# Kernel tuning notes

Measured on AMD Instinct MI355X. Metric: run time of the kernel, lower is better.

Reference implementation:

```python
import jax, jax.numpy as jnp
import numpy as np

EPS = 1e-12

def _l2norm(v, axis=-1):
    n = jnp.sqrt(jnp.sum(v * v, axis=axis, keepdims=True))
    return v / jnp.maximum(n, EPS)

def setup_inputs() -> dict:
    key = jax.random.key(0)
    ks = jax.random.split(key, 6)
    B, S, E, A = 256, 128, 768, 30
    x = jax.random.normal(ks[0], (B, S, E), dtype=jnp.float32)
    W_att = jax.random.normal(ks[1], (E, E), dtype=jnp.float32) * (1.0 / np.sqrt(E))
    b_att = jnp.zeros((E,), dtype=jnp.float32)
    W_red = jax.random.normal(ks[2], (E, A), dtype=jnp.float32) * (1.0 / np.sqrt(E))
    b_red = jnp.zeros((A,), dtype=jnp.float32)
    aspect_W = jax.random.normal(ks[3], (A, E), dtype=jnp.float32) * (1.0 / np.sqrt(E))
    # negatives: uniform over other batch elements (multinomial on ones - eye)
    idx = jax.random.randint(ks[4], (B, 10), 0, B - 1)
    neg_idx = (idx + (idx >= jnp.arange(B)[:, None])).astype(jnp.int32)  # skip self
    return {"x": x, "W_att": W_att, "b_att": b_att, "W_red": W_red,
            "b_red": b_red, "aspect_W": aspect_W, "neg_idx": neg_idx}

def reference(x, W_att, b_att, W_red, b_red, aspect_W, neg_idx):
    # --- LuongAttention(general): query = mean over seq ---
    q = x.mean(axis=1)                                   # [B,E]
    qW = q @ W_att + b_att                               # [B,E]
    scores = jnp.einsum('bse,be->bs', x, qW)             # [B,S]
    attn = jax.nn.softmax(scores, axis=-1)
    z_s = jnp.einsum('bs,bse->be', attn, x)              # attended sentence vec [B,E]
    # --- reduction + reconstruction ---
    composition = jax.nn.softmax(z_s @ W_red + b_red, axis=-1)  # [B,A]
    reconstructed = composition @ aspect_W                      # [B,E]
    # --- max-margin loss with gathered negatives ---
    r_s = _l2norm(reconstructed)                         # F.normalize
    z_n = z_s[neg_idx]                                   # [B,10,E] gather
    pos = jnp.einsum('be,be->b', z_s, r_s)[:, None]      # [B,1]
    negs = jnp.einsum('bne,be->bn', z_n, r_s)            # [B,10]
    J = 1.0 - pos + negs
    margin_loss = jnp.mean(jnp.maximum(J, 0.0))
    # --- orthogonal regularization on aspect embeddings ---
    T_n = _l2norm(aspect_W, axis=1)                      # [A,E]
    G = T_n @ T_n.T - jnp.eye(aspect_W.shape[0], dtype=aspect_W.dtype)
    reg = jnp.sqrt(jnp.sum(G * G))                       # Frobenius norm
    loss = reg + margin_loss
    return (z_s, reconstructed, loss)
```

## Files before the change

kernel.cpp:

```cpp
#include <hip/hip_runtime.h>
#include <hip/hip_bf16.h>
#include <math.h>

#define B 256
#define S 128
#define E 768
#define E4 192
#define NA 30
#define NNEG 10

#define K2_KC 96
#define K2_KR 192

__device__ __forceinline__ float dot4(float4 a, float4 b) {
    return a.x * b.x + a.y * b.y + a.z * b.z + a.w * b.w;
}
__device__ __forceinline__ float wave_reduce_sum(float v) {
#pragma unroll
    for (int off = 32; off; off >>= 1) v += __shfl_down(v, off);
    return v;
}
__device__ __forceinline__ float wave_reduce_max(float v) {
#pragma unroll
    for (int off = 32; off; off >>= 1) v = fmaxf(v, __shfl_down(v, off));
    return v;
}

__global__ __launch_bounds__(768) void mean_prep_kernel(const float* __restrict__ x,
                                                        const float* __restrict__ W_red,
                                                        const float* __restrict__ aspect_W,
                                                        float* __restrict__ q,
                                                        float* __restrict__ WredT,
                                                        float* __restrict__ invn) {
    int bid = blockIdx.x;
    int tid = threadIdx.x;
    __shared__ __align__(16) float4 part[4][E4];
    __shared__ float red[12];

    if (bid < 2 * B) {
        int b = bid >> 1, half = bid & 1;
        int c = tid % E4;
        int g = tid / E4;
        const float4* xb = (const float4*)(x + (size_t)b * S * E);
        int s0 = half * 64 + g * 16;
        float4 acc = make_float4(0.f, 0.f, 0.f, 0.f);
#pragma unroll 4
        for (int s = s0; s < s0 + 16; ++s) {
            float4 v = xb[(size_t)s * E4 + c];
            acc.x += v.x; acc.y += v.y; acc.z += v.z; acc.w += v.w;
        }
        part[g][c] = acc;
        __syncthreads();
        if (tid < E4) {
            float4 a0 = part[0][c], a1 = part[1][c], a2 = part[2][c], a3 = part[3][c];
            const float inv = 1.0f / (float)S;
            float4 r;
            r.x = (a0.x + a1.x + a2.x + a3.x) * inv;
            r.y = (a0.y + a1.y + a2.y + a3.y) * inv;
            r.z = (a0.z + a1.z + a2.z + a3.z) * inv;
            r.w = (a0.w + a1.w + a2.w + a3.w) * inv;
            ((float4*)q)[((size_t)half * B + b) * E4 + c] = r;
        }
    } else {
        int a = bid - 2 * B;
        WredT[(size_t)a * E + tid] = W_red[(size_t)tid * NA + a];
        int wave = tid >> 6, lane = tid & 63;
        float v = aspect_W[(size_t)a * E + tid];
        float ss = wave_reduce_sum(v * v);
        if (lane == 0) red[wave] = ss;
        __syncthreads();
        if (tid == 0) {
            float n = 0.f;
#pragma unroll
            for (int w = 0; w < 12; ++w) n += red[w];
            invn[a] = 1.0f / fmaxf(sqrtf(n), 1e-12f);
        }
    }
}

__global__ __launch_bounds__(256) void qw_partial_kernel(const float* __restrict__ q,
                                                         const float* __restrict__ W_att,
                                                         float* __restrict__ part) {
    int b0 = blockIdx.x * 64;
    int e0 = blockIdx.y * 64;
    int kz = blockIdx.z;
    int k0 = kz * K2_KR;
    int tid = threadIdx.x;

    __shared__ __align__(16) float qs[64][K2_KC + 4];
    __shared__ __align__(16) float ws[K2_KC][64];

    int r0 = (tid >> 3) * 2;
    int c0 = (tid & 7) * 8;

    float4 a00 = make_float4(0,0,0,0), a01 = make_float4(0,0,0,0);
    float4 a10 = make_float4(0,0,0,0), a11 = make_float4(0,0,0,0);

    for (int ch = 0; ch < 2; ++ch) {
        int kc0 = k0 + ch * K2_KC;
        {
            int row = tid >> 2, ks = (tid & 3) * 24;
            const float* src0 = q + (size_t)(b0 + row) * E + kc0 + ks;
            const float* src1 = src0 + (size_t)B * E;
#pragma unroll
            for (int j = 0; j < 6; ++j) {
                float4 v0 = *(const float4*)(src0 + 4 * j);
                float4 v1 = *(const float4*)(src1 + 4 * j);
                v0.x += v1.x; v0.y += v1.y; v0.z += v1.z; v0.w += v1.w;
                *(float4*)&qs[row][ks + 4 * j] = v0;
            }
        }
        for (int i = tid; i < K2_KC * 16; i += 256) {
            int row = i >> 4, e4 = (i & 15) * 4;
            *(float4*)&ws[row][e4] =
                *(const float4*)(W_att + (size_t)(kc0 + row) * E + e0 + e4);
        }
        __syncthreads();
#pragma unroll 4
        for (int k = 0; k < K2_KC; ++k) {
            float qa = qs[r0][k], qb = qs[r0 + 1][k];
            float4 w0 = *(const float4*)&ws[k][c0];
            float4 w1 = *(const float4*)&ws[k][c0 + 4];
            a00.x += qa * w0.x; a00.y += qa * w0.y; a00.z += qa * w0.z; a00.w += qa * w0.w;
            a01.x += qa * w1.x; a01.y += qa * w1.y; a01.z += qa * w1.z; a01.w += qa * w1.w;
            a10.x += qb * w0.x; a10.y += qb * w0.y; a10.z += qb * w0.z; a10.w += qb * w0.w;
            a11.x += qb * w1.x; a11.y += qb * w1.y; a11.z += qb * w1.z; a11.w += qb * w1.w;
        }
        __syncthreads();
    }
    float* dst = part + ((size_t)kz * B + b0 + r0) * E + e0 + c0;
    *(float4*)dst = a00; *(float4*)(dst + 4) = a01;
    *(float4*)(dst + E) = a10; *(float4*)(dst + E + 4) = a11;
}

__global__ __launch_bounds__(768) void attn_ortho_kernel(const float* __restrict__ x,
                                                         const float* __restrict__ part,
                                                         const float* __restrict__ b_att,
                                                         const float* __restrict__ aspect_W,
                                                         const float* __restrict__ invn,
                                                         float* __restrict__ z_s,
                                                         float* __restrict__ Gpart) {
    int bid = blockIdx.x;
    int tid = threadIdx.x, wave = tid >> 6, lane = tid & 63;
    __shared__ __align__(16) float4 qw4[E4];
    __shared__ float att[S];
    __shared__ float red[12];
    __shared__ __align__(16) float4 zpart[4][E4];

    if (bid >= B) {
        int i = bid - B;
        float inv_i = invn[i];
        if (tid < E4) {
            float4 v = ((const float4*)aspect_W)[(size_t)i * E4 + tid];
            v.x *= inv_i; v.y *= inv_i; v.z *= inv_i; v.w *= inv_i;
            qw4[tid] = v;
        }
        __syncthreads();
        float acc = 0.f;
        for (int j = wave; j < NA; j += 12) {
            const float4* aj = (const float4*)(aspect_W + (size_t)j * E);
            float d = 0.f;
#pragma unroll
            for (int jj = 0; jj < 3; ++jj)
                d += dot4(aj[lane + 64 * jj], qw4[lane + 64 * jj]);
            d = wave_reduce_sum(d);
            if (lane == 0) {
                float g = d * invn[j] - ((i == j) ? 1.f : 0.f);
                acc += g * g;
            }
        }
        if (lane == 0) red[wave] = acc;
        __syncthreads();
        if (tid == 0) {
            float s = 0.f;
#pragma unroll
            for (int w = 0; w < 12; ++w) s += red[w];
            Gpart[i] = s;
        }
        return;
    }

    int b = bid;
    const int N4 = B * E / 4;
    if (tid < E4) {
        const float4* p = (const float4*)part;
        size_t base = (size_t)b * E4 + tid;
        float4 s0 = p[base], s1 = p[base + N4], s2 = p[base + 2 * N4], s3 = p[base + 3 * N4];
        float4 bb = ((const float4*)b_att)[tid];
        float4 r;
        r.x = s0.x + s1.x + s2.x + s3.x + bb.x;
        r.y = s0.y + s1.y + s2.y + s3.y + bb.y;
        r.z = s0.z + s1.z + s2.z + s3.z + bb.z;
        r.w = s0.w + s1.w + s2.w + s3.w + bb.w;
        qw4[tid] = r;
    }
    __syncthreads();

    const float4* xb = (const float4*)(x + (size_t)b * S * E);

    for (int p2 = wave; p2 < S / 2; p2 += 12) {
        int sA = 2 * p2;
        const float4* rA = xb + (size_t)sA * E4;
        const float4* rB = rA + E4;
        float dA = 0.f, dB = 0.f;
#pragma unroll
        for (int j = 0; j < 3; ++j) {
            float4 qv = qw4[lane + 64 * j];
            dA += dot4(rA[lane + 64 * j], qv);
            dB += dot4(rB[lane + 64 * j], qv);
        }
#pragma unroll
        for (int off = 32; off; off >>= 1) {
            dA += __shfl_down(dA, off);
            dB += __shfl_down(dB, off);
        }
        if (lane == 0) { att[sA] = dA; att[sA + 1] = dB; }
    }
    __syncthreads();

    float v = (tid < S) ? att[tid] : -3.4e38f;
    if (tid < S) {
        float m = wave_reduce_max(v);
        if (lane == 0) red[wave] = m;
    }
    __syncthreads();
    float gm = fmaxf(red[0], red[1]);
    float ex = 0.f;
    if (tid < S) {
        ex = expf(v - gm);
        float ss = wave_reduce_sum(ex);
        if (lane == 0) red[4 + wave] = ss;
    }
    __syncthreads();
    float tot = red[4] + red[5];
    if (tid < S) att[tid] = ex / tot;
    __syncthreads();

    int c = tid % E4, g = tid / E4;
    float4 acc = make_float4(0.f, 0.f, 0.f, 0.f);
#pragma unroll 4
    for (int s = g * 32 + 31; s >= g * 32; --s) {
        float w = att[s];
        float4 xv = xb[(size_t)s * E4 + c];
        acc.x += w * xv.x; acc.y += w * xv.y; acc.z += w * xv.z; acc.w += w * xv.w;
    }
    zpart[g][c] = acc;
    __syncthreads();
    if (tid < E4) {
        float4 a0 = zpart[0][tid], a1 = zpart[1][tid], a2 = zpart[2][tid], a3 = zpart[3][tid];
        float4 r;
        r.x = a0.x + a1.x + a2.x + a3.x;
        r.y = a0.y + a1.y + a2.y + a3.y;
        r.z = a0.z + a1.z + a2.z + a3.z;
        r.w = a0.w + a1.w + a2.w + a3.w;
        ((float4*)z_s)[(size_t)b * E4 + tid] = r;
    }
}

__global__ __launch_bounds__(256) void recon_margin_kernel(const float* __restrict__ z_s,
                                                           const float* __restrict__ WredT,
                                                           const float* __restrict__ b_red,
                                                           const float* __restrict__ aspect_W,
                                                           const int* __restrict__ neg_idx,
                                                           float* __restrict__ recon,
                                                           float* __restrict__ mpart) {
    int b = blockIdx.x;
    int tid = threadIdx.x, wave = tid >> 6, lane = tid & 63;
    __shared__ __align__(16) float4 z4[E4];
    __shared__ float comp[NA];
    __shared__ __align__(16) float r_sh[E];
    __shared__ float red[4];
    __shared__ float dots[12];

    if (tid < E4) z4[tid] = ((const float4*)(z_s + (size_t)b * E))[tid];
    __syncthreads();

    for (int a = wave; a < NA; a += 4) {
        const float4* wr = (const float4*)(WredT + (size_t)a * E);
        float d = 0.f;
#pragma unroll
        for (int j = 0; j < 3; ++j)
            d += dot4(wr[lane + 64 * j], z4[lane + 64 * j]);
        d = wave_reduce_sum(d);
        if (lane == 0) comp[a] = d + b_red[a];
    }
    __syncthreads();

    if (wave == 0) {
        float v = (lane < NA) ? comp[lane] : -3.4e38f;
        float m = wave_reduce_max(v);
        m = __shfl(m, 0);
        float e = (lane < NA) ? expf(v - m) : 0.f;
        float ssum = wave_reduce_sum(e);
        ssum = __shfl(ssum, 0);
        if (lane < NA) comp[lane] = e / ssum;
    }
    __syncthreads();

    float r0 = 0.f, r1 = 0.f, r2 = 0.f;
    for (int a = 0; a < NA; ++a) {
        float cm = comp[a];
        const float* ar = aspect_W + (size_t)a * E;
        r0 += cm * ar[tid];
        r1 += cm * ar[tid + 256];
        r2 += cm * ar[tid + 512];
    }
    float* rb = recon + (size_t)b * E;
    rb[tid] = r0; rb[tid + 256] = r1; rb[tid + 512] = r2;
    r_sh[tid] = r0; r_sh[tid + 256] = r1; r_sh[tid + 512] = r2;
    float sq = r0 * r0 + r1 * r1 + r2 * r2;
    sq = wave_reduce_sum(sq);
    if (lane == 0) red[wave] = sq;
    __syncthreads();
    float inv = 1.0f / fmaxf(sqrtf(red[0] + red[1] + red[2] + red[3]), 1e-12f);

    for (int d = wave; d < NNEG + 1; d += 4) {
        int row = (d == 0) ? b : neg_idx[b * NNEG + (d - 1)];
        const float4* zr = (const float4*)(z_s + (size_t)row * E);
        const float4* rr = (const float4*)r_sh;
        float acc = 0.f;
#pragma unroll
        for (int j = 0; j < 3; ++j)
            acc += dot4(zr[lane + 64 * j], rr[lane + 64 * j]);
        acc = wave_reduce_sum(acc);
        if (lane == 0) dots[d] = acc;
    }
    __syncthreads();
    if (tid == 0) {
        float pos = dots[0] * inv;
        float ssum = 0.f;
        for (int n = 1; n <= NNEG; ++n)
            ssum += fmaxf(1.f - pos + dots[n] * inv, 0.f);
        mpart[b] = ssum;
    }
}

__global__ __launch_bounds__(256) void loss_kernel(const float* __restrict__ Gpart,
                                                   const float* __restrict__ mpart,
                                                   float* __restrict__ loss_out) {
    int tid = threadIdx.x, wave = tid >> 6, lane = tid & 63;
    __shared__ float ra[4], rb[4];
    float fr = (tid < NA) ? Gpart[tid] : 0.f;
    fr = wave_reduce_sum(fr);
    if (lane == 0) ra[wave] = fr;
    float mp = mpart[tid];
    mp = wave_reduce_sum(mp);
    if (lane == 0) rb[wave] = mp;
    __syncthreads();
    if (tid == 0) {
        float frob = sqrtf(ra[0] + ra[1] + ra[2] + ra[3]);
        float msum = rb[0] + rb[1] + rb[2] + rb[3];
        loss_out[0] = frob + msum * (1.0f / (float)(B * NNEG));
    }
}

extern "C" void kernel_launch(void* const* d_in, const int* in_sizes, int n_in,
                              void* d_out, int out_size, void* d_ws, size_t ws_size,
                              hipStream_t stream) {
    const float* x        = (const float*)d_in[0];
    const float* W_att    = (const float*)d_in[1];
    const float* b_att    = (const float*)d_in[2];
    const float* W_red    = (const float*)d_in[3];
    const float* b_red    = (const float*)d_in[4];
    const float* aspect_W = (const float*)d_in[5];
    const int*   neg_idx  = (const int*)d_in[6];

    float* out   = (float*)d_out;
    float* z_s   = out;
    float* recon = out + (size_t)B * E;
    float* loss  = out + (size_t)2 * B * E;

    float* ws    = (float*)d_ws;
    float* q     = ws;
    float* part2 = q + (size_t)2 * B * E;
    float* WredT = part2 + (size_t)4 * B * E;
    float* invn  = WredT + (size_t)NA * E;
    float* Gpart = invn + 32;
    float* mpart = Gpart + 32;

    mean_prep_kernel<<<2 * B + NA, 768, 0, stream>>>(x, W_red, aspect_W, q, WredT, invn);
    qw_partial_kernel<<<dim3(4, 12, 4), 256, 0, stream>>>(q, W_att, part2);
    attn_ortho_kernel<<<B + NA, 768, 0, stream>>>(x, part2, b_att, aspect_W, invn, z_s, Gpart);
    recon_margin_kernel<<<B, 256, 0, stream>>>(z_s, WredT, b_red, aspect_W, neg_idx, recon, mpart);
    loss_kernel<<<1, 256, 0, stream>>>(Gpart, mpart, loss);
}
```

Baseline: 77.81 us.

## Fuse mean and qW GEMV into one kernel; fold loss into recon via ticket

New measurement: 126.6 us. 1.63x slower.

```diff
diff --git a/kernel.cpp b/kernel.cpp
--- a/kernel.cpp
+++ b/kernel.cpp
@@ -9,9 +9,6 @@
 #define NA 30
 #define NNEG 10
 
-#define K2_KC 96
-#define K2_KR 192
-
 __device__ __forceinline__ float dot4(float4 a, float4 b) {
     return a.x * b.x + a.y * b.y + a.z * b.z + a.w * b.w;
 }
@@ -26,43 +23,22 @@
     return v;
 }
 
-__global__ __launch_bounds__(768) void mean_prep_kernel(const float* __restrict__ x,
-                                                        const float* __restrict__ W_red,
-                                                        const float* __restrict__ aspect_W,
-                                                        float* __restrict__ q,
-                                                        float* __restrict__ WredT,
-                                                        float* __restrict__ invn) {
+__global__ __launch_bounds__(768) void meanqw_prep_kernel(const float* __restrict__ x,
+                                                          const float* __restrict__ W_att,
+                                                          const float* __restrict__ W_red,
+                                                          const float* __restrict__ aspect_W,
+                                                          float* __restrict__ part,
+                                                          float* __restrict__ WredT,
+                                                          float* __restrict__ invn,
+                                                          unsigned int* __restrict__ counter) {
     int bid = blockIdx.x;
     int tid = threadIdx.x;
-    __shared__ __align__(16) float4 part[4][E4];
+    __shared__ __align__(16) float4 qp4[4][8][24];
+    __shared__ __align__(16) float qs[8][100];
     __shared__ float red[12];
 
-    if (bid < 2 * B) {
-        int b = bid >> 1, half = bid & 1;
-        int c = tid % E4;
-        int g = tid / E4;
-        const float4* xb = (const float4*)(x + (size_t)b * S * E);
-        int s0 = half * 64 + g * 16;
-        float4 acc = make_float4(0.f, 0.f, 0.f, 0.f);
-#pragma unroll 4
-        for (int s = s0; s < s0 + 16; ++s) {
-            float4 v = xb[(size_t)s * E4 + c];
-            acc.x += v.x; acc.y += v.y; acc.z += v.z; acc.w += v.w;
-        }
-        part[g][c] = acc;
-        __syncthreads();
-        if (tid < E4) {
-            float4 a0 = part[0][c], a1 = part[1][c], a2 = part[2][c], a3 = part[3][c];
-            const float inv = 1.0f / (float)S;
-            float4 r;
-            r.x = (a0.x + a1.x + a2.x + a3.x) * inv;
-            r.y = (a0.y + a1.y + a2.y + a3.y) * inv;
-            r.z = (a0.z + a1.z + a2.z + a3.z) * inv;
-            r.w = (a0.w + a1.w + a2.w + a3.w) * inv;
-            ((float4*)q)[((size_t)half * B + b) * E4 + c] = r;
-        }
-    } else {
-        int a = bid - 2 * B;
+    if (bid >= 256) {
+        int a = bid - 256;
         WredT[(size_t)a * E + tid] = W_red[(size_t)tid * NA + a];
         int wave = tid >> 6, lane = tid & 63;
         float v = aspect_W[(size_t)a * E + tid];
@@ -75,62 +51,58 @@
             for (int w = 0; w < 12; ++w) n += red[w];
             invn[a] = 1.0f / fmaxf(sqrtf(n), 1e-12f);
         }
-    }
-}
-
-__global__ __launch_bounds__(256) void qw_partial_kernel(const float* __restrict__ q,
-                                                         const float* __restrict__ W_att,
-                                                         float* __restrict__ part) {
-    int b0 = blockIdx.x * 64;
-    int e0 = blockIdx.y * 64;
-    int kz = blockIdx.z;
-    int k0 = kz * K2_KR;
-    int tid = threadIdx.x;
-
-    __shared__ __align__(16) float qs[64][K2_KC + 4];
-    __shared__ __align__(16) float ws[K2_KC][64];
-
-    int r0 = (tid >> 3) * 2;
-    int c0 = (tid & 7) * 8;
-
-    float4 a00 = make_float4(0,0,0,0), a01 = make_float4(0,0,0,0);
-    float4 a10 = make_float4(0,0,0,0), a11 = make_float4(0,0,0,0);
-
-    for (int ch = 0; ch < 2; ++ch) {
-        int kc0 = k0 + ch * K2_KC;
-        {
-            int row = tid >> 2, ks = (tid & 3) * 24;
-            const float* src0 = q + (size_t)(b0 + row) * E + kc0 + ks;
-            const float* src1 = src0 + (size_t)B * E;
-#pragma unroll
-            for (int j = 0; j < 6; ++j) {
-                float4 v0 = *(const float4*)(src0 + 4 * j);
-                float4 v1 = *(const float4*)(src1 + 4 * j);
-                v0.x += v1.x; v0.y += v1.y; v0.z += v1.z; v0.w += v1.w;
-                *(float4*)&qs[row][ks + 4 * j] = v0;
-            }
-        }
-        for (int i = tid; i < K2_KC * 16; i += 256) {
-            int row = i >> 4, e4 = (i & 15) * 4;
-            *(float4*)&ws[row][e4] =
-                *(const float4*)(W_att + (size_t)(kc0 + row) * E + e0 + e4);
-        }
-        __syncthreads();
+        return;
+    }
+
+    if (bid == 0 && tid == 0) *counter = 0u;
+
+    int bt = bid >> 3, kt = bid & 7;
+    int b0 = bt * 8, k0 = kt * 96;
+
+    int c  = tid % 24;
+    int bi = (tid / 24) & 7;
+    int g  = tid / 192;
+    const float4* xrow = (const float4*)(x + (size_t)(b0 + bi) * S * E) + (k0 >> 2) + c;
+    float4 acc = make_float4(0.f, 0.f, 0.f, 0.f);
+#pragma unroll 8
+    for (int s = g * 32; s < g * 32 + 32; ++s) {
+        float4 v = xrow[(size_t)s * E4];
+        acc.x += v.x; acc.y += v.y; acc.z += v.z; acc.w += v.w;
+    }
+    qp4[g][bi][c] = acc;
+    __syncthreads();
+    if (tid < 192) {
+        int bj = tid / 24, cc = tid % 24;
+        float4 a0 = qp4[0][bj][cc], a1 = qp4[1][bj][cc], a2 = qp4[2][bj][cc], a3 = qp4[3][bj][cc];
+        const float inv = 1.0f / (float)S;
+        float4 r;
+        r.x = (a0.x + a1.x + a2.x + a3.x) * inv;
+        r.y = (a0.y + a1.y + a2.y + a3.y) * inv;
+        r.z = (a0.z + a1.z + a2.z + a3.z) * inv;
+        r.w = (a0.w + a1.w + a2.w + a3.w) * inv;
+        *(float4*)&qs[bj][cc * 4] = r;
+    }
+    __syncthreads();
+
+    int bj = tid / 96;
+    int e0 = (tid % 96) * 8;
+    float4 o0 = make_float4(0.f, 0.f, 0.f, 0.f), o1 = make_float4(0.f, 0.f, 0.f, 0.f);
+    const float* Wb = W_att + (size_t)k0 * E + e0;
 #pragma unroll 4
-        for (int k = 0; k < K2_KC; ++k) {
-            float qa = qs[r0][k], qb = qs[r0 + 1][k];
-            float4 w0 = *(const float4*)&ws[k][c0];
-            float4 w1 = *(const float4*)&ws[k][c0 + 4];
-            a00.x += qa * w0.x; a00.y += qa * w0.y; a00.z += qa * w0.z; a00.w += qa * w0.w;
-            a01.x += qa * w1.x; a01.y += qa * w1.y; a01.z += qa * w1.z; a01.w += qa * w1.w;
-            a10.x += qb * w0.x; a10.y += qb * w0.y; a10.z += qb * w0.z; a10.w += qb * w0.w;
-            a11.x += qb * w1.x; a11.y += qb * w1.y; a11.z += qb * w1.z; a11.w += qb * w1.w;
-        }
-        __syncthreads();
-    }
-    float* dst = part + ((size_t)kz * B + b0 + r0) * E + e0 + c0;
-    *(float4*)dst = a00; *(float4*)(dst + 4) = a01;
-    *(float4*)(dst + E) = a10; *(float4*)(dst + E + 4) = a11;
+    for (int kk = 0; kk < 24; ++kk) {
+        float4 q4 = *(const float4*)&qs[bj][kk * 4];
+#pragma unroll
+        for (int j = 0; j < 4; ++j) {
+            const float* wr = Wb + (size_t)(kk * 4 + j) * E;
+            float4 w0 = *(const float4*)wr;
+            float4 w1 = *(const float4*)(wr + 4);
+            float qv = (j == 0) ? q4.x : (j == 1) ? q4.y : (j == 2) ? q4.z : q4.w;
+            o0.x += qv * w0.x; o0.y += qv * w0.y; o0.z += qv * w0.z; o0.w += qv * w0.w;
+            o1.x += qv * w1.x; o1.y += qv * w1.y; o1.z += qv * w1.z; o1.w += qv * w1.w;
+        }
+    }
+    float* dst = part + ((size_t)kt * B + b0 + bj) * E + e0;
+    *(float4*)dst = o0; *(float4*)(dst + 4) = o1;
 }
 
 __global__ __launch_bounds__(768) void attn_ortho_kernel(const float* __restrict__ x,
@@ -185,13 +157,12 @@
     if (tid < E4) {
         const float4* p = (const float4*)part;
         size_t base = (size_t)b * E4 + tid;
-        float4 s0 = p[base], s1 = p[base + N4], s2 = p[base + 2 * N4], s3 = p[base + 3 * N4];
-        float4 bb = ((const float4*)b_att)[tid];
-        float4 r;
-        r.x = s0.x + s1.x + s2.x + s3.x + bb.x;
-        r.y = s0.y + s1.y + s2.y + s3.y + bb.y;
-        r.z = s0.z + s1.z + s2.z + s3.z + bb.z;
-        r.w = s0.w + s1.w + s2.w + s3.w + bb.w;
+        float4 r = ((const float4*)b_att)[tid];
+#pragma unroll
+        for (int i = 0; i < 8; ++i) {
+            float4 s = p[base + (size_t)i * N4];
+            r.x += s.x; r.y += s.y; r.z += s.z; r.w += s.w;
+        }
         qw4[tid] = r;
     }
     __syncthreads();
@@ -257,25 +228,29 @@
     }
 }
 
-__global__ __launch_bounds__(256) void recon_margin_kernel(const float* __restrict__ z_s,
-                                                           const float* __restrict__ WredT,
-                                                           const float* __restrict__ b_red,
-                                                           const float* __restrict__ aspect_W,
-                                                           const int* __restrict__ neg_idx,
-                                                           float* __restrict__ recon,
-                                                           float* __restrict__ mpart) {
+__global__ __launch_bounds__(768) void recon_margin_loss_kernel(const float* __restrict__ z_s,
+                                                                const float* __restrict__ WredT,
+                                                                const float* __restrict__ b_red,
+                                                                const float* __restrict__ aspect_W,
+                                                                const int* __restrict__ neg_idx,
+                                                                const float* __restrict__ Gpart,
+                                                                float* __restrict__ recon,
+                                                                float* __restrict__ mpart,
+                                                                unsigned int* __restrict__ counter,
+                                                                float* __restrict__ loss_out) {
     int b = blockIdx.x;
     int tid = threadIdx.x, wave = tid >> 6, lane = tid & 63;
     __shared__ __align__(16) float4 z4[E4];
     __shared__ float comp[NA];
     __shared__ __align__(16) float r_sh[E];
-    __shared__ float red[4];
+    __shared__ float red[12];
     __shared__ float dots[12];
+    __shared__ unsigned int ticket;
 
     if (tid < E4) z4[tid] = ((const float4*)(z_s + (size_t)b * E))[tid];
     __syncthreads();
 
-    for (int a = wave; a < NA; a += 4) {
+    for (int a = wave; a < NA; a += 12) {
         const float4* wr = (const float4*)(WredT + (size_t)a * E);
         float d = 0.f;
 #pragma unroll
@@ -297,25 +272,21 @@
     }
     __syncthreads();
 
-    float r0 = 0.f, r1 = 0.f, r2 = 0.f;
-    for (int a = 0; a < NA; ++a) {
-        float cm = comp[a];
-        const float* ar = aspect_W + (size_t)a * E;
-        r0 += cm * ar[tid];
-        r1 += cm * ar[tid + 256];
-        r2 += cm * ar[tid + 512];
-    }
-    float* rb = recon + (size_t)b * E;
-    rb[tid] = r0; rb[tid + 256] = r1; rb[tid + 512] = r2;
-    r_sh[tid] = r0; r_sh[tid + 256] = r1; r_sh[tid + 512] = r2;
-    float sq = r0 * r0 + r1 * r1 + r2 * r2;
-    sq = wave_reduce_sum(sq);
+    float r = 0.f;
+    for (int a = 0; a < NA; ++a)
+        r += comp[a] * aspect_W[(size_t)a * E + tid];
+    recon[(size_t)b * E + tid] = r;
+    r_sh[tid] = r;
+    float sq = wave_reduce_sum(r * r);
     if (lane == 0) red[wave] = sq;
     __syncthreads();
-    float inv = 1.0f / fmaxf(sqrtf(red[0] + red[1] + red[2] + red[3]), 1e-12f);
-
-    for (int d = wave; d < NNEG + 1; d += 4) {
-        int row = (d == 0) ? b : neg_idx[b * NNEG + (d - 1)];
+    float tot = 0.f;
+#pragma unroll
+    for (int w = 0; w < 12; ++w) tot += red[w];
+    float inv = 1.0f / fmaxf(sqrtf(tot), 1e-12f);
+
+    if (wave <= NNEG) {
+        int row = (wave == 0) ? b : neg_idx[b * NNEG + (wave - 1)];
         const float4* zr = (const float4*)(z_s + (size_t)row * E);
         const float4* rr = (const float4*)r_sh;
         float acc = 0.f;
@@ -323,7 +294,7 @@
         for (int j = 0; j < 3; ++j)
             acc += dot4(zr[lane + 64 * j], rr[lane + 64 * j]);
         acc = wave_reduce_sum(acc);
-        if (lane == 0) dots[d] = acc;
+        if (lane == 0) dots[wave] = acc;
     }
     __syncthreads();
     if (tid == 0) {
@@ -333,24 +304,25 @@
             ssum += fmaxf(1.f - pos + dots[n] * inv, 0.f);
         mpart[b] = ssum;
     }
-}
-
-__global__ __launch_bounds__(256) void loss_kernel(const float* __restrict__ Gpart,
-                                                   const float* __restrict__ mpart,
-                                                   float* __restrict__ loss_out) {
-    int tid = threadIdx.x, wave = tid >> 6, lane = tid & 63;
-    __shared__ float ra[4], rb[4];
-    float fr = (tid < NA) ? Gpart[tid] : 0.f;
-    fr = wave_reduce_sum(fr);
-    if (lane == 0) ra[wave] = fr;
-    float mp = mpart[tid];
-    mp = wave_reduce_sum(mp);
-    if (lane == 0) rb[wave] = mp;
-    __syncthreads();
-    if (tid == 0) {
-        float frob = sqrtf(ra[0] + ra[1] + ra[2] + ra[3]);
-        float msum = rb[0] + rb[1] + rb[2] + rb[3];
-        loss_out[0] = frob + msum * (1.0f / (float)(B * NNEG));
+
+    __threadfence();
+    if (tid == 0) ticket = atomicAdd(counter, 1u);
+    __syncthreads();
+    if (ticket == B - 1) {
+        __threadfence();
+        float mp = (tid < B) ? mpart[tid] : 0.f;
+        mp = wave_reduce_sum(mp);
+        if (lane == 0) red[wave] = mp;
+        float gp = (tid < NA) ? Gpart[tid] : 0.f;
+        gp = wave_reduce_sum(gp);
+        if (lane == 0) dots[wave] = gp;
+        __syncthreads();
+        if (tid == 0) {
+            float ms = 0.f, fr = 0.f;
+#pragma unroll
+            for (int w = 0; w < 12; ++w) { ms += red[w]; fr += dots[w]; }
+            loss_out[0] = sqrtf(fr) + ms * (1.0f / (float)(B * NNEG));
+        }
     }
 }
 
@@ -371,16 +343,16 @@
     float* loss  = out + (size_t)2 * B * E;
 
     float* ws    = (float*)d_ws;
-    float* q     = ws;
-    float* part2 = q + (size_t)2 * B * E;
-    float* WredT = part2 + (size_t)4 * B * E;
+    float* part2 = ws;
+    float* WredT = part2 + (size_t)8 * B * E;
     float* invn  = WredT + (size_t)NA * E;
     float* Gpart = invn + 32;
     float* mpart = Gpart + 32;
-
-    mean_prep_kernel<<<2 * B + NA, 768, 0, stream>>>(x, W_red, aspect_W, q, WredT, invn);
-    qw_partial_kernel<<<dim3(4, 12, 4), 256, 0, stream>>>(q, W_att, part2);
+    unsigned int* counter = (unsigned int*)(mpart + B);
+
+    meanqw_prep_kernel<<<256 + NA, 768, 0, stream>>>(x, W_att, W_red, aspect_W,
+                                                     part2, WredT, invn, counter);
     attn_ortho_kernel<<<B + NA, 768, 0, stream>>>(x, part2, b_att, aspect_W, invn, z_s, Gpart);
-    recon_margin_kernel<<<B, 256, 0, stream>>>(z_s, WredT, b_red, aspect_W, neg_idx, recon, mpart);
-    loss_kernel<<<1, 256, 0, stream>>>(Gpart, mpart, loss);
-}
+    recon_margin_loss_kernel<<<B, 768, 0, stream>>>(z_s, WredT, b_red, aspect_W, neg_idx,
+                                                    Gpart, recon, mpart, counter, loss);
+}
```

## Fuse final loss reduction into recon kernel via last-block atomic ticket

Applied to the files above, without the earlier changes.

New measurement: 122.8 us. 1.58x slower.

```diff
diff --git a/kernel.cpp b/kernel.cpp
--- a/kernel.cpp
+++ b/kernel.cpp
@@ -31,11 +31,14 @@
                                                         const float* __restrict__ aspect_W,
                                                         float* __restrict__ q,
                                                         float* __restrict__ WredT,
-                                                        float* __restrict__ invn) {
+                                                        float* __restrict__ invn,
+                                                        unsigned int* __restrict__ counter) {
     int bid = blockIdx.x;
     int tid = threadIdx.x;
     __shared__ __align__(16) float4 part[4][E4];
     __shared__ float red[12];
+
+    if (bid == 0 && tid == 0) *counter = 0u;
 
     if (bid < 2 * B) {
         int b = bid >> 1, half = bid & 1;
@@ -257,25 +260,29 @@
     }
 }
 
-__global__ __launch_bounds__(256) void recon_margin_kernel(const float* __restrict__ z_s,
-                                                           const float* __restrict__ WredT,
-                                                           const float* __restrict__ b_red,
-                                                           const float* __restrict__ aspect_W,
-                                                           const int* __restrict__ neg_idx,
-                                                           float* __restrict__ recon,
-                                                           float* __restrict__ mpart) {
+__global__ __launch_bounds__(768) void recon_margin_loss_kernel(const float* __restrict__ z_s,
+                                                                const float* __restrict__ WredT,
+                                                                const float* __restrict__ b_red,
+                                                                const float* __restrict__ aspect_W,
+                                                                const int* __restrict__ neg_idx,
+                                                                const float* __restrict__ Gpart,
+                                                                float* __restrict__ recon,
+                                                                float* __restrict__ mpart,
+                                                                unsigned int* __restrict__ counter,
+                                                                float* __restrict__ loss_out) {
     int b = blockIdx.x;
     int tid = threadIdx.x, wave = tid >> 6, lane = tid & 63;
     __shared__ __align__(16) float4 z4[E4];
     __shared__ float comp[NA];
     __shared__ __align__(16) float r_sh[E];
-    __shared__ float red[4];
+    __shared__ float red[12];
     __shared__ float dots[12];
+    __shared__ unsigned int ticket;
 
     if (tid < E4) z4[tid] = ((const float4*)(z_s + (size_t)b * E))[tid];
     __syncthreads();
 
-    for (int a = wave; a < NA; a += 4) {
+    for (int a = wave; a < NA; a += 12) {
         const float4* wr = (const float4*)(WredT + (size_t)a * E);
         float d = 0.f;
 #pragma unroll
@@ -297,25 +304,21 @@
     }
     __syncthreads();
 
-    float r0 = 0.f, r1 = 0.f, r2 = 0.f;
-    for (int a = 0; a < NA; ++a) {
-        float cm = comp[a];
-        const float* ar = aspect_W + (size_t)a * E;
-        r0 += cm * ar[tid];
-        r1 += cm * ar[tid + 256];
-        r2 += cm * ar[tid + 512];
-    }
-    float* rb = recon + (size_t)b * E;
-    rb[tid] = r0; rb[tid + 256] = r1; rb[tid + 512] = r2;
-    r_sh[tid] = r0; r_sh[tid + 256] = r1; r_sh[tid + 512] = r2;
-    float sq = r0 * r0 + r1 * r1 + r2 * r2;
-    sq = wave_reduce_sum(sq);
+    float r = 0.f;
+    for (int a = 0; a < NA; ++a)
+        r += comp[a] * aspect_W[(size_t)a * E + tid];
+    recon[(size_t)b * E + tid] = r;
+    r_sh[tid] = r;
+    float sq = wave_reduce_sum(r * r);
     if (lane == 0) red[wave] = sq;
     __syncthreads();
-    float inv = 1.0f / fmaxf(sqrtf(red[0] + red[1] + red[2] + red[3]), 1e-12f);
-
-    for (int d = wave; d < NNEG + 1; d += 4) {
-        int row = (d == 0) ? b : neg_idx[b * NNEG + (d - 1)];
+    float tot = 0.f;
+#pragma unroll
+    for (int w = 0; w < 12; ++w) tot += red[w];
+    float inv = 1.0f / fmaxf(sqrtf(tot), 1e-12f);
+
+    if (wave <= NNEG) {
+        int row = (wave == 0) ? b : neg_idx[b * NNEG + (wave - 1)];
         const float4* zr = (const float4*)(z_s + (size_t)row * E);
         const float4* rr = (const float4*)r_sh;
         float acc = 0.f;
@@ -323,7 +326,7 @@
         for (int j = 0; j < 3; ++j)
             acc += dot4(zr[lane + 64 * j], rr[lane + 64 * j]);
         acc = wave_reduce_sum(acc);
-        if (lane == 0) dots[d] = acc;
+        if (lane == 0) dots[wave] = acc;
     }
     __syncthreads();
     if (tid == 0) {
@@ -333,24 +336,25 @@
             ssum += fmaxf(1.f - pos + dots[n] * inv, 0.f);
         mpart[b] = ssum;
     }
-}
-
-__global__ __launch_bounds__(256) void loss_kernel(const float* __restrict__ Gpart,
-                                                   const float* __restrict__ mpart,
-                                                   float* __restrict__ loss_out) {
-    int tid = threadIdx.x, wave = tid >> 6, lane = tid & 63;
-    __shared__ float ra[4], rb[4];
-    float fr = (tid < NA) ? Gpart[tid] : 0.f;
-    fr = wave_reduce_sum(fr);
-    if (lane == 0) ra[wave] = fr;
-    float mp = mpart[tid];
-    mp = wave_reduce_sum(mp);
-    if (lane == 0) rb[wave] = mp;
-    __syncthreads();
-    if (tid == 0) {
-        float frob = sqrtf(ra[0] + ra[1] + ra[2] + ra[3]);
-        float msum = rb[0] + rb[1] + rb[2] + rb[3];
-        loss_out[0] = frob + msum * (1.0f / (float)(B * NNEG));
+
+    __threadfence();
+    if (tid == 0) ticket = atomicAdd(counter, 1u);
+    __syncthreads();
+    if (ticket == B - 1) {
+        __threadfence();
+        float mp = (tid < B) ? mpart[tid] : 0.f;
+        mp = wave_reduce_sum(mp);
+        if (lane == 0) red[wave] = mp;
+        float gp = (tid < NA) ? Gpart[tid] : 0.f;
+        gp = wave_reduce_sum(gp);
+        if (lane == 0) dots[wave] = gp;
+        __syncthreads();
+        if (tid == 0) {
+            float ms = 0.f, fr = 0.f;
+#pragma unroll
+            for (int w = 0; w < 12; ++w) { ms += red[w]; fr += dots[w]; }
+            loss_out[0] = sqrtf(fr) + ms * (1.0f / (float)(B * NNEG));
+        }
     }
 }
 
@@ -377,10 +381,11 @@
     float* invn  = WredT + (size_t)NA * E;
     float* Gpart = invn + 32;
     float* mpart = Gpart + 32;
-
-    mean_prep_kernel<<<2 * B + NA, 768, 0, stream>>>(x, W_red, aspect_W, q, WredT, invn);
+    unsigned int* counter = (unsigned int*)(mpart + B);
+
+    mean_prep_kernel<<<2 * B + NA, 768, 0, stream>>>(x, W_red, aspect_W, q, WredT, invn, counter);
     qw_partial_kernel<<<dim3(4, 12, 4), 256, 0, stream>>>(q, W_att, part2);
     attn_ortho_kernel<<<B + NA, 768, 0, stream>>>(x, part2, b_att, aspect_W, invn, z_s, Gpart);
-    recon_margin_kernel<<<B, 256, 0, stream>>>(z_s, WredT, b_red, aspect_W, neg_idx, recon, mpart);
-    loss_kernel<<<1, 256, 0, stream>>>(Gpart, mpart, loss);
-}
+    recon_margin_loss_kernel<<<B, 768, 0, stream>>>(z_s, WredT, b_red, aspect_W, neg_idx,
+                                                    Gpart, recon, mpart, counter, loss);
+}
```
